# Optimization experiments

Measured on AMD Instinct MI355X. Metric: run time of the kernel, lower is better.

## Reference

```python
import jax, jax.numpy as jnp
import numpy as np

N, M, D0, D1, H, E = 1024, 4096, 1024, 512, 512, 64
TAU = 0.5


def setup_inputs() -> dict:
    key = jax.random.key(0)
    ks = jax.random.split(key, 24)
    g = lambda k, shape, s=0.05: (jax.random.normal(k, shape, jnp.float32) * s)
    # 0/1 meta-path neighbor incidence matrices, avg degree ~16
    nei0 = (jax.random.uniform(ks[0], (N, M)) < 0.004).astype(jnp.float32)
    nei1 = (jax.random.uniform(ks[1], (N, M)) < 0.004).astype(jnp.float32)
    def norm_adj(k):
        a = (jax.random.uniform(k, (N, N)) < 0.005).astype(jnp.float32) + jnp.eye(N, dtype=jnp.float32)
        return a / a.sum(1, keepdims=True)
    return dict(
        feat0=g(ks[2], (N, D0), 1.0), feat1=g(ks[3], (M, D1), 1.0), feat2=g(ks[4], (M, D1), 1.0),
        mask_feat=g(ks[5], (N, D0), 1.0),
        nei0=nei0, nei1=nei1,
        adj0=norm_adj(ks[6]), adj1=norm_adj(ks[7]),
        madj0=norm_adj(ks[8]), madj1=norm_adj(ks[9]),
        fc0_w=g(ks[10], (D0, H)), fc0_b=jnp.zeros((H,), jnp.float32),
        fc1_w=g(ks[11], (D1, H)), fc1_b=jnp.zeros((H,), jnp.float32),
        fc2_w=g(ks[12], (D1, H)), fc2_b=jnp.zeros((H,), jnp.float32),
        agg0_w=g(ks[13], (H, H)), agg1_w=g(ks[14], (H, H)),
        gcn_w1=g(ks[15], (H, E)), gcn_b1=jnp.zeros((E,), jnp.float32),
        gcn_w2=g(ks[16], (E, E)), gcn_b2=jnp.zeros((E,), jnp.float32),
        att_w=g(ks[17], (E, E)), att_b=jnp.zeros((E,), jnp.float32),
        att_vec=g(ks[18], (E,)),
        proj_w=g(ks[19], (E, E)), proj_b=jnp.zeros((E,), jnp.float32),
        mlp1_w=g(ks[20], (E, 16)), mlp1_b=jnp.zeros((16,), jnp.float32),
        mlp2_w=g(ks[21], (16, 1)), mlp2_b=jnp.zeros((1,), jnp.float32),
    )


def _l2norm(x):
    # F.normalize(dim=1)
    return x / jnp.maximum(jnp.linalg.norm(x, axis=1, keepdims=True), 1e-12)


def reference(feat0, feat1, feat2, mask_feat, nei0, nei1, adj0, adj1, madj0, madj1,
              fc0_w, fc0_b, fc1_w, fc1_b, fc2_w, fc2_b, agg0_w, agg1_w,
              gcn_w1, gcn_b1, gcn_w2, gcn_b2, att_w, att_b, att_vec,
              proj_w, proj_b, mlp1_w, mlp1_b, mlp2_w, mlp2_b):
    elu = jax.nn.elu
    # aggregate_nei_acm (dropout in eval mode => identity)
    h_tar = elu(feat0 @ fc0_w + fc0_b)                       # [N, H]
    h_mask = elu(mask_feat @ fc0_w + fc0_b)                  # [N, H]
    h_nei = [elu(feat1 @ fc1_w + fc1_b), elu(feat2 @ fc2_w + fc2_b)]  # [M, H]
    neis = [nei0, nei1]
    agg_ws = [agg0_w, agg1_w]
    views, masks = [], []
    for i in range(2):
        cnt = jnp.maximum(neis[i].sum(1, keepdims=True), 1.0)  # nei_index_count, clamped >0
        h_agg = (neis[i] @ h_nei[i]) / cnt                     # sparse neighbor mean, [N, H]
        t = h_agg @ agg_ws[i]
        views.append(elu(h_tar + t))
        masks.append(elu(h_mask + t))

    def gcn(x, adj):
        # 2-layer GCN: relu(A X W1 + b1) -> A H W2 + b2
        h = jax.nn.relu(adj @ (x @ gcn_w1) + gcn_b1)
        return adj @ (h @ gcn_w2) + gcn_b2

    mean_adj = (adj0 + adj1) * 0.5                           # torch.stack(adjs).mean(0)
    z_coarse = gcn(h_tar, mean_adj)                          # [N, E]
    # order: Encoder(view_i, adj_i), Encoder(mask_i, mask_adj_i) per i
    h_fine = [gcn(views[0], adj0), gcn(masks[0], madj0),
              gcn(views[1], adj1), gcn(masks[1], madj1)]
    hs = jnp.stack([_l2norm(h) for h in h_fine])             # [V=4, N, E]
    # semantic attention over views
    e = jnp.einsum('vne,e->v', jnp.tanh(hs @ att_w + att_b), att_vec) / hs.shape[1]
    beta = jax.nn.softmax(e)
    z_fine = jnp.einsum('v,vne->ne', beta, hs)               # [N, E]
    zc = _l2norm(jnp.tanh(z_coarse @ proj_w + proj_b))
    zf = _l2norm(jnp.tanh(z_fine @ proj_w + proj_b))
    # weight_InfoNce
    logits = (zf @ zc.T) / TAU                               # [N, N]
    dots = jnp.exp(logits)
    pair = zf[:, None, :] + zc[None, :, :]                   # [N, N, E] = z_anchor[i] + z[j]
    w = jax.nn.sigmoid(jnp.tanh(pair @ mlp1_w + mlp1_b) @ mlp2_w + mlp2_b)[..., 0]
    denom = jnp.sum(dots * w, axis=1)
    # -log(diag(dots)/denom) = log(denom) - diag(logits)
    loss = jnp.mean(jnp.log(denom) - jnp.diagonal(logits))
    return loss
```

## Files before the change

### kernel.cpp

```cpp
#include <hip/hip_runtime.h>

#define ACT_NONE 0
#define ACT_ELU  1
#define ACT_RELU 2
#define ACT_TANH 3

typedef __attribute__((ext_vector_type(8))) short short8;
typedef __attribute__((ext_vector_type(4))) float f32x4;

__device__ __forceinline__ float frcp(float x) { return __builtin_amdgcn_rcpf(x); }
__device__ __forceinline__ float fexp(float x) { return __expf(x); }
__device__ __forceinline__ float ftanh(float x) {
    return 1.f - 2.f * frcp(fexp(2.f * x) + 1.f);
}
__device__ __forceinline__ float fsigmoid(float x) {
    return frcp(1.f + fexp(-x));
}

__device__ __forceinline__ float apply_act(float v, int act) {
    if (act == ACT_ELU)  return v > 0.f ? v : fexp(v) - 1.f;
    if (act == ACT_RELU) return fmaxf(v, 0.f);
    if (act == ACT_TANH) return ftanh(v);
    return v;
}

__device__ __forceinline__ unsigned short f2bf(float f) {
    unsigned int u = __float_as_uint(f);
    unsigned int r = (u + 0x7fffu + ((u >> 16) & 1u)) >> 16;
    return (unsigned short)r;
}
__device__ __forceinline__ float bf2f(unsigned short u) {
    return __uint_as_float(((unsigned int)u) << 16);
}

struct CMDesc { const float* in; unsigned short* out; int start4; };
struct CMArr { CMDesc d[6]; int n; int total4; };

__global__ __launch_bounds__(256) void cast_multi_kernel(CMArr a) {
    int g4 = blockIdx.x * 256 + threadIdx.x;
    if (g4 >= a.total4) return;
    int s = 0;
    while (s + 1 < a.n && g4 >= a.d[s + 1].start4) ++s;
    int l4 = g4 - a.d[s].start4;
    float4 v = *reinterpret_cast<const float4*>(a.d[s].in + (size_t)l4 * 4);
    ushort4 o;
    o.x = f2bf(v.x); o.y = f2bf(v.y); o.z = f2bf(v.z); o.w = f2bf(v.w);
    *reinterpret_cast<ushort4*>(a.d[s].out + (size_t)l4 * 4) = o;
}

struct CTDesc { const float* in; unsigned short* out; int R, C, tcols, tile0; };
struct CTArr { CTDesc d[10]; int n; };

__global__ void castT_multi_kernel(CTArr a) {
    int b = blockIdx.x, s = 0;
    while (s + 1 < a.n && b >= a.d[s + 1].tile0) ++s;
    const CTDesc d = a.d[s];
    int lt = b - d.tile0;
    int tr = lt / d.tcols, tc = lt % d.tcols;
    int r0 = tr * 32, c0 = tc * 32;
    __shared__ float t[32][33];
    int tx = threadIdx.x, ty = threadIdx.y;
    for (int i = ty; i < 32; i += 8) {
        int r = r0 + i, c = c0 + tx;
        t[i][tx] = (r < d.R && c < d.C) ? d.in[(size_t)r * d.C + c] : 0.f;
    }
    __syncthreads();
    for (int i = ty; i < 32; i += 8) {
        int c = c0 + i, r = r0 + tx;
        if (c < d.C && r < d.R) d.out[(size_t)c * d.R + r] = f2bf(t[tx][i]);
    }
}

__global__ __launch_bounds__(256) void gemm_bf16_kernel(
    const unsigned short* __restrict__ A, const unsigned short* __restrict__ Bt,
    const unsigned short* __restrict__ Bt2, int m_split,
    const float* __restrict__ bias, const float* __restrict__ bias2,
    float* __restrict__ C, unsigned short* __restrict__ Cbf, int cbf_mlimit,
    int M, int K, int N, int act) {
    const int tid = threadIdx.x;
    const int w = tid >> 6, lane = tid & 63;
    const int wr = w >> 1, wc = w & 1;
    const int lr = lane & 15, lk = lane >> 4;
    const int bm = blockIdx.y * 64, bn = blockIdx.x * 64;
    const unsigned short* Bu = Bt;
    const float* bu = bias;
    if (bm >= m_split) { Bu = Bt2; bu = bias2; }

    const int arow0 = bm + wr * 32 + lr;
    const int brow0 = bn + wc * 32 + lr;

    f32x4 acc[2][2] = {};
    const short8 zero8 = {};
    #pragma unroll 4
    for (int k0 = 0; k0 < K; k0 += 32) {
        short8 a[2], b[2];
        #pragma unroll
        for (int i = 0; i < 2; ++i)
            a[i] = *reinterpret_cast<const short8*>(&A[(size_t)(arow0 + i * 16) * K + k0 + lk * 8]);
        #pragma unroll
        for (int j = 0; j < 2; ++j) {
            int br = brow0 + j * 16;
            b[j] = (br < N) ? *reinterpret_cast<const short8*>(&Bu[(size_t)br * K + k0 + lk * 8])
                            : zero8;
        }
        #pragma unroll
        for (int i = 0; i < 2; ++i)
            #pragma unroll
            for (int j = 0; j < 2; ++j)
                acc[i][j] = __builtin_amdgcn_mfma_f32_16x16x32_bf16(a[i], b[j], acc[i][j], 0, 0, 0);
    }
    #pragma unroll
    for (int i = 0; i < 2; ++i) {
        #pragma unroll
        for (int j = 0; j < 2; ++j) {
            int gcol = bn + wc * 32 + j * 16 + lr;
            if (gcol >= N) continue;
            float bv = bu ? bu[gcol] : 0.f;
            #pragma unroll
            for (int r = 0; r < 4; ++r) {
                int grow = bm + wr * 32 + i * 16 + lk * 4 + r;
                float v = apply_act(acc[i][j][r] + bv, act);
                if (C)   C[(size_t)grow * N + gcol] = v;
                if (Cbf && grow < cbf_mlimit) Cbf[(size_t)grow * N + gcol] = f2bf(v);
            }
        }
    }
}

__global__ __launch_bounds__(256) void neiagg_kernel(
    const float* __restrict__ nei0, const float* __restrict__ nei1,
    const unsigned short* __restrict__ hn0, const unsigned short* __restrict__ hn1,
    unsigned short* __restrict__ hagg) {
    const int row = blockIdx.x, br = blockIdx.y, t = threadIdx.x;
    const float* nei = br ? nei1 : nei0;
    const unsigned short* hn = br ? hn1 : hn0;
    __shared__ int idxs[256];
    __shared__ int cnt;
    if (t == 0) cnt = 0;
    __syncthreads();
    const float4* nr = reinterpret_cast<const float4*>(nei + (size_t)row * 4096);
    for (int j = t; j < 1024; j += 256) {
        float4 v = nr[j];
        if (v.x != 0.f) { int s = atomicAdd(&cnt, 1); if (s < 256) idxs[s] = j * 4 + 0; }
        if (v.y != 0.f) { int s = atomicAdd(&cnt, 1); if (s < 256) idxs[s] = j * 4 + 1; }
        if (v.z != 0.f) { int s = atomicAdd(&cnt, 1); if (s < 256) idxs[s] = j * 4 + 2; }
        if (v.w != 0.f) { int s = atomicAdd(&cnt, 1); if (s < 256) idxs[s] = j * 4 + 3; }
    }
    __syncthreads();
    int n = cnt < 256 ? cnt : 256;
    float inv = frcp(fmaxf((float)cnt, 1.f));
    int c = t * 2;
    float a0 = 0.f, a1 = 0.f, b0 = 0.f, b1 = 0.f;
    int k = 0;
    for (; k + 2 <= n; k += 2) {
        ushort2 u = *reinterpret_cast<const ushort2*>(&hn[(size_t)idxs[k] * 512 + c]);
        ushort2 v = *reinterpret_cast<const ushort2*>(&hn[(size_t)idxs[k + 1] * 512 + c]);
        a0 += bf2f(u.x); a1 += bf2f(u.y);
        b0 += bf2f(v.x); b1 += bf2f(v.y);
    }
    if (k < n) {
        ushort2 u = *reinterpret_cast<const ushort2*>(&hn[(size_t)idxs[k] * 512 + c]);
        a0 += bf2f(u.x); a1 += bf2f(u.y);
    }
    ushort2 o; o.x = f2bf((a0 + b0) * inv); o.y = f2bf((a1 + b1) * inv);
    *reinterpret_cast<ushort2*>(&hagg[((size_t)br * 1024 + row) * 512 + c]) = o;
}

__global__ void addelu_kernel(const float* __restrict__ ht, const float* __restrict__ hm,
                              const float* __restrict__ tt, unsigned short* __restrict__ xcat,
                              int nh) {
    int idx = blockIdx.x * 256 + threadIdx.x;
    if (idx < nh) {
        float h1 = ht[idx], h2 = hm[idx];
        float t0 = tt[idx], t1 = tt[idx + nh];
        float a = h1 + t0, b = h2 + t0, c = h1 + t1, d = h2 + t1;
        xcat[(size_t)1 * nh + idx] = f2bf(a > 0.f ? a : fexp(a) - 1.f);
        xcat[(size_t)2 * nh + idx] = f2bf(b > 0.f ? b : fexp(b) - 1.f);
        xcat[(size_t)3 * nh + idx] = f2bf(c > 0.f ? c : fexp(c) - 1.f);
        xcat[(size_t)4 * nh + idx] = f2bf(d > 0.f ? d : fexp(d) - 1.f);
    }
}

__global__ __launch_bounds__(64) void adjprep_kernel(
    const float* __restrict__ adj0, const float* __restrict__ adj1,
    const float* __restrict__ madj0, const float* __restrict__ madj1,
    int* __restrict__ cnts, int* __restrict__ idxs, float* __restrict__ wts) {
    const int row = blockIdx.x, br = blockIdx.y, t = threadIdx.x;
    const float* Aa; const float* Ab = nullptr; float sc = 1.f;
    if (br == 0)      { Aa = adj0; Ab = adj1; sc = 0.5f; }
    else if (br == 1) { Aa = adj0; }
    else if (br == 2) { Aa = madj0; }
    else if (br == 3) { Aa = adj1; }
    else              { Aa = madj1; }
    __shared__ int li[128];
    __shared__ float lw[128];
    __shared__ int cnt;
    if (t == 0) cnt = 0;
    __syncthreads();
    const float4* ar = reinterpret_cast<const float4*>(Aa + (size_t)row * 1024);
    const float4* brp = Ab ? reinterpret_cast<const float4*>(Ab + (size_t)row * 1024) : nullptr;
    for (int j = t; j < 256; j += 64) {
        float4 v = ar[j];
        if (brp) { float4 u = brp[j]; v.x += u.x; v.y += u.y; v.z += u.z; v.w += u.w; }
        if (v.x != 0.f) { int s = atomicAdd(&cnt, 1); if (s < 128) { li[s] = j * 4 + 0; lw[s] = v.x * sc; } }
        if (v.y != 0.f) { int s = atomicAdd(&cnt, 1); if (s < 128) { li[s] = j * 4 + 1; lw[s] = v.y * sc; } }
        if (v.z != 0.f) { int s = atomicAdd(&cnt, 1); if (s < 128) { li[s] = j * 4 + 2; lw[s] = v.z * sc; } }
        if (v.w != 0.f) { int s = atomicAdd(&cnt, 1); if (s < 128) { li[s] = j * 4 + 3; lw[s] = v.w * sc; } }
    }
    __syncthreads();
    int n = cnt < 128 ? cnt : 128;
    size_t base = ((size_t)br * 1024 + row) * 128;
    for (int k = t; k < n; k += 64) { idxs[base + k] = li[k]; wts[base + k] = lw[k]; }
    if (t == 0) cnts[br * 1024 + row] = n;
}

__device__ __forceinline__ float sparse_gather(const int* __restrict__ idxs,
                                               const float* __restrict__ wts,
                                               size_t base, int n,
                                               const float* __restrict__ Xb, int t,
                                               float acc) {
    float a1 = 0.f, a2 = 0.f, a3 = 0.f;
    int k = 0;
    for (; k + 4 <= n; k += 4) {
        int   i0 = idxs[base + k],     i1 = idxs[base + k + 1];
        int   i2 = idxs[base + k + 2], i3 = idxs[base + k + 3];
        float w0 = wts[base + k],      w1 = wts[base + k + 1];
        float w2 = wts[base + k + 2],  w3 = wts[base + k + 3];
        acc += w0 * Xb[(size_t)i0 * 64 + t];
        a1  += w1 * Xb[(size_t)i1 * 64 + t];
        a2  += w2 * Xb[(size_t)i2 * 64 + t];
        a3  += w3 * Xb[(size_t)i3 * 64 + t];
    }
    for (; k < n; ++k) acc += wts[base + k] * Xb[(size_t)idxs[base + k] * 64 + t];
    return acc + a1 + a2 + a3;
}

__global__ __launch_bounds__(64) void spmm1_kernel(
    const int* __restrict__ cnts, const int* __restrict__ idxs, const float* __restrict__ wts,
    const float* __restrict__ X, const float* __restrict__ bias,
    unsigned short* __restrict__ out) {
    const int row = blockIdx.x, br = blockIdx.y, t = threadIdx.x;
    size_t base = ((size_t)br * 1024 + row) * 128;
    int n = cnts[br * 1024 + row];
    float acc = sparse_gather(idxs, wts, base, n, X + (size_t)br * 1024 * 64, t, bias[t]);
    out[((size_t)br * 1024 + row) * 64 + t] = f2bf(fmaxf(acc, 0.f));
}

__global__ __launch_bounds__(64) void spmm2_kernel(
    const int* __restrict__ cnts, const int* __restrict__ idxs, const float* __restrict__ wts,
    const float* __restrict__ X, const float* __restrict__ bias,
    unsigned short* __restrict__ zcf_bf, float* __restrict__ hs,
    const float* __restrict__ att_w, const float* __restrict__ att_b,
    const float* __restrict__ att_vec, float* __restrict__ att_row) {
    const int row = blockIdx.x, br = blockIdx.y, t = threadIdx.x;
    size_t base = ((size_t)br * 1024 + row) * 128;
    int n = cnts[br * 1024 + row];
    float acc = sparse_gather(idxs, wts, base, n, X + (size_t)br * 1024 * 64, t, bias[t]);
    if (br == 0) {
        zcf_bf[(size_t)row * 64 + t] = f2bf(acc);
        return;
    }
    float s = acc * acc;
    #pragma unroll
    for (int o = 32; o; o >>= 1) s += __shfl_down(s, o);
    s = __shfl(s, 0);
    float v = acc * frcp(fmaxf(sqrtf(s), 1e-12f));
    hs[((size_t)(br - 1) * 1024 + row) * 64 + t] = v;
    __shared__ float rs[64];
    rs[t] = v;
    __syncthreads();
    float sa = att_b[t];
    #pragma unroll
    for (int k = 0; k < 64; ++k) sa += rs[k] * att_w[k * 64 + t];
    float val = ftanh(sa) * att_vec[t];
    #pragma unroll
    for (int o = 32; o; o >>= 1) val += __shfl_down(val, o);
    if (t == 0) att_row[(size_t)(br - 1) * 1024 + row] = val;
}

__global__ __launch_bounds__(256) void attreduce_kernel(const float* __restrict__ att_row,
                                                        float* __restrict__ small) {
    const int v = blockIdx.x, t = threadIdx.x;
    const float* p = att_row + (size_t)v * 1024;
    float s = p[t] + p[t + 256] + p[t + 512] + p[t + 768];
    #pragma unroll
    for (int o = 32; o; o >>= 1) s += __shfl_down(s, o);
    __shared__ float ps[4];
    if ((t & 63) == 0) ps[t >> 6] = s;
    __syncthreads();
    if (t == 0) small[v] = ps[0] + ps[1] + ps[2] + ps[3];
}

__global__ void zfine_kernel(const float* __restrict__ hs, const float* __restrict__ small,
                             unsigned short* __restrict__ out) {
    int idx = blockIdx.x * 256 + threadIdx.x;
    if (idx < 65536) {
        float e0 = small[0] * (1.f / 1024.f), e1 = small[1] * (1.f / 1024.f);
        float e2 = small[2] * (1.f / 1024.f), e3 = small[3] * (1.f / 1024.f);
        float mx = fmaxf(fmaxf(e0, e1), fmaxf(e2, e3));
        float x0 = expf(e0 - mx), x1 = expf(e1 - mx), x2 = expf(e2 - mx), x3 = expf(e3 - mx);
        float inv = 1.f / (x0 + x1 + x2 + x3);
        float v = (x0 * hs[idx] + x1 * hs[idx + 65536] +
                   x2 * hs[idx + 131072] + x3 * hs[idx + 196608]) * inv;
        out[idx] = f2bf(v);
    }
}

__global__ __launch_bounds__(64) void l2normcast_kernel(float* __restrict__ X,
                                                        unsigned short* __restrict__ Xbf) {
    const int row = blockIdx.x, t = threadIdx.x;
    float v = X[(size_t)row * 64 + t];
    float s = v * v;
    #pragma unroll
    for (int o = 32; o; o >>= 1) s += __shfl_down(s, o);
    s = __shfl(s, 0);
    float r = v * frcp(fmaxf(sqrtf(s), 1e-12f));
    X[(size_t)row * 64 + t] = r;
    Xbf[(size_t)row * 64 + t] = f2bf(r);
}

__global__ __launch_bounds__(256) void infonce_kernel(
    const float* __restrict__ zf, const float* __restrict__ zc,
    const float* __restrict__ A1, const float* __restrict__ C1,
    const float* __restrict__ b1, const float* __restrict__ m2,
    const float* __restrict__ b2v, float* __restrict__ loss_acc) {
    const int i0 = blockIdx.x * 4, t = threadIdx.x;
    __shared__ __align__(16) float zfs[4][64];
    __shared__ float a1b[4][16], m2s[16];
    __shared__ float diag[4];
    __shared__ float wsum[4][4];
    if (t < 64) {
        #pragma unroll
        for (int ii = 0; ii < 4; ++ii) zfs[ii][t] = zf[(size_t)(i0 + ii) * 64 + t];
    }
    if (t < 16) {
        float bb = b1[t];
        #pragma unroll
        for (int ii = 0; ii < 4; ++ii) a1b[ii][t] = A1[(size_t)(i0 + ii) * 16 + t] + bb;
        m2s[t] = m2[t];
    }
    __syncthreads();
    const float b2 = b2v[0];
    float acc[4] = {};
    for (int j = t; j < 1024; j += 256) {
        const float4* zcj = reinterpret_cast<const float4*>(zc + (size_t)j * 64);
        float dot[4] = {};
        #pragma unroll
        for (int e = 0; e < 16; ++e) {
            float4 b = zcj[e];
            #pragma unroll
            for (int ii = 0; ii < 4; ++ii) {
                float4 a = reinterpret_cast<const float4*>(zfs[ii])[e];
                dot[ii] += a.x * b.x + a.y * b.y + a.z * b.z + a.w * b.w;
            }
        }
        float c1j[16];
        #pragma unroll
        for (int q = 0; q < 4; ++q) {
            float4 c4 = reinterpret_cast<const float4*>(C1 + (size_t)j * 16)[q];
            c1j[q * 4 + 0] = c4.x; c1j[q * 4 + 1] = c4.y;
            c1j[q * 4 + 2] = c4.z; c1j[q * 4 + 3] = c4.w;
        }
        #pragma unroll
        for (int ii = 0; ii < 4; ++ii) {
            float logit = dot[ii] * 2.0f;
            float h = b2;
            #pragma unroll
            for (int k = 0; k < 16; ++k) h += ftanh(a1b[ii][k] + c1j[k]) * m2s[k];
            acc[ii] += fexp(logit) * fsigmoid(h);
            if (j == i0 + ii) diag[ii] = logit;
        }
    }
    #pragma unroll
    for (int ii = 0; ii < 4; ++ii) {
        float a = acc[ii];
        #pragma unroll
        for (int o = 32; o; o >>= 1) a += __shfl_down(a, o);
        if ((t & 63) == 0) wsum[t >> 6][ii] = a;
    }
    __syncthreads();
    if (t == 0) {
        float part = 0.f;
        #pragma unroll
        for (int ii = 0; ii < 4; ++ii) {
            float denom = wsum[0][ii] + wsum[1][ii] + wsum[2][ii] + wsum[3][ii];
            part += logf(denom) - diag[ii];
        }
        atomicAdd(loss_acc, part);
    }
}

__global__ void finalize_kernel(const float* __restrict__ small, float* __restrict__ out) {
    if (threadIdx.x == 0) out[0] = small[4] * (1.f / 1024.f);
}

extern "C" void kernel_launch(void* const* d_in, const int* in_sizes, int n_in,
                              void* d_out, int out_size, void* d_ws, size_t ws_size,
                              hipStream_t stream) {
    const float* feat0     = (const float*)d_in[0];
    const float* feat1     = (const float*)d_in[1];
    const float* feat2     = (const float*)d_in[2];
    const float* mask_feat = (const float*)d_in[3];
    const float* nei0      = (const float*)d_in[4];
    const float* nei1      = (const float*)d_in[5];
    const float* adj0      = (const float*)d_in[6];
    const float* adj1      = (const float*)d_in[7];
    const float* madj0     = (const float*)d_in[8];
    const float* madj1     = (const float*)d_in[9];
    const float* fc0_w = (const float*)d_in[10];
    const float* fc0_b = (const float*)d_in[11];
    const float* fc1_w = (const float*)d_in[12];
    const float* fc1_b = (const float*)d_in[13];
    const float* fc2_w = (const float*)d_in[14];
    const float* fc2_b = (const float*)d_in[15];
    const float* agg0_w = (const float*)d_in[16];
    const float* agg1_w = (const float*)d_in[17];
    const float* gcn_w1 = (const float*)d_in[18];
    const float* gcn_b1 = (const float*)d_in[19];
    const float* gcn_w2 = (const float*)d_in[20];
    const float* gcn_b2 = (const float*)d_in[21];
    const float* att_w  = (const float*)d_in[22];
    const float* att_b  = (const float*)d_in[23];
    const float* att_vec = (const float*)d_in[24];
    const float* proj_w = (const float*)d_in[25];
    const float* proj_b = (const float*)d_in[26];
    const float* mlp1_w = (const float*)d_in[27];
    const float* mlp1_b = (const float*)d_in[28];
    const float* mlp2_w = (const float*)d_in[29];
    const float* mlp2_b = (const float*)d_in[30];

    const int N = 1024, M = 4096, D0 = 1024, D1 = 512, H = 512, E = 64;
    typedef unsigned short bf;

    float* W = (float*)d_ws;
    size_t off = 0;
    auto allocf = [&](size_t n) { float* p = W + off; off += n; return p; };
    float* h_tar   = allocf((size_t)N * H);
    float* h_mask  = allocf((size_t)N * H);
    float* tbuf    = allocf((size_t)2 * N * H);
    float* xw1cat  = allocf((size_t)5 * N * E);
    float* hw2cat  = allocf((size_t)5 * N * E);
    float* hs      = allocf((size_t)4 * N * E);
    float* zcat    = allocf((size_t)2 * N * E);
    float* AC1     = allocf((size_t)2 * N * 16);
    float* att_row = allocf((size_t)4 * N);
    float* small   = allocf(16);
    float* adj_wts = allocf((size_t)5 * 1024 * 128);
    int*   adj_idx = (int*)allocf((size_t)5 * 1024 * 128);
    int*   adj_cnt = (int*)allocf((size_t)5 * 1024);
    bf* BP = (bf*)(W + off);
    size_t boff = 0;
    auto allocb = [&](size_t n) { bf* p = BP + boff; boff += n; return p; };
    bf* feat0_bf = allocb((size_t)N * D0);
    bf* mask_bf  = allocb((size_t)N * D0);
    bf* feat1_bf = allocb((size_t)M * D1);
    bf* feat2_bf = allocb((size_t)M * D1);
    bf* xcat_bf  = allocb((size_t)5 * N * H);
    bf* hnei0_bf = allocb((size_t)M * H);
    bf* hnei1_bf = allocb((size_t)M * H);
    bf* hagg_bf  = allocb((size_t)2 * N * H);
    bf* h1cat_bf = allocb((size_t)5 * N * E);
    bf* zcf_bf   = allocb((size_t)2 * N * E);
    bf* zcat_bf  = allocb((size_t)2 * N * E);
    bf* fc0_wT  = allocb((size_t)H * D0);
    bf* fc1_wT  = allocb((size_t)H * D1);
    bf* fc2_wT  = allocb((size_t)H * D1);
    bf* agg0_wT = allocb((size_t)H * H);
    bf* agg1_wT = allocb((size_t)H * H);
    bf* gw1_T   = allocb((size_t)E * H);
    bf* gw2_T   = allocb((size_t)E * E);
    bf* proj_wT = allocb((size_t)E * E);
    bf* mlp1_wT = allocb((size_t)16 * E);

    auto gemm = [&](const bf* A, const bf* Bt, const bf* Bt2, int msplit,
                    const float* bias, const float* bias2, float* C, bf* Cbf, int cbf_lim,
                    int Mm, int Kk, int Nn, int act) {
        dim3 g((Nn + 63) / 64, Mm / 64);
        gemm_bf16_kernel<<<g, 256, 0, stream>>>(A, Bt, Bt2, msplit, bias, bias2,
                                                C, Cbf, cbf_lim, Mm, Kk, Nn, act);
    };

    hipMemsetAsync((void*)small, 0, 16 * sizeof(float), stream);

    {
        CTArr a; int tile = 0, i = 0;
        auto add = [&](const float* in, bf* out, int R, int C) {
            int tc = (C + 31) / 32, trn = (R + 31) / 32;
            a.d[i++] = CTDesc{in, out, R, C, tc, tile};
            tile += tc * trn;
        };
        add(fc0_w, fc0_wT, D0, H);
        add(fc1_w, fc1_wT, D1, H);
        add(fc2_w, fc2_wT, D1, H);
        add(agg0_w, agg0_wT, H, H);
        add(agg1_w, agg1_wT, H, H);
        add(gcn_w1, gw1_T, H, E);
        add(gcn_w2, gw2_T, E, E);
        add(proj_w, proj_wT, E, E);
        add(mlp1_w, mlp1_wT, E, 16);
        a.n = i;
        castT_multi_kernel<<<tile, dim3(32, 8), 0, stream>>>(a);
    }
    {
        CMArr a; int s4 = 0, i = 0;
        auto add = [&](const float* in, bf* out, int n) {
            a.d[i++] = CMDesc{in, out, s4}; s4 += n / 4;
        };
        add(feat0, feat0_bf, N * D0);
        add(mask_feat, mask_bf, N * D0);
        add(feat1, feat1_bf, M * D1);
        add(feat2, feat2_bf, M * D1);
        a.n = i; a.total4 = s4;
        cast_multi_kernel<<<(s4 + 255) / 256, 256, 0, stream>>>(a);
    }
    adjprep_kernel<<<dim3(N, 5), 64, 0, stream>>>(adj0, adj1, madj0, madj1,
                                                  adj_cnt, adj_idx, adj_wts);

    gemm(feat0_bf, fc0_wT, nullptr, 1 << 30, fc0_b, nullptr,
         h_tar, xcat_bf, N, 2 * N, D0, H, ACT_ELU);
    gemm(feat1_bf, fc1_wT, fc2_wT, M, fc1_b, fc2_b,
         nullptr, hnei0_bf, 2 * M, 2 * M, D1, H, ACT_ELU);

    neiagg_kernel<<<dim3(N, 2), 256, 0, stream>>>(nei0, nei1, hnei0_bf, hnei1_bf, hagg_bf);
    gemm(hagg_bf, agg0_wT, agg1_wT, N, nullptr, nullptr,
         tbuf, nullptr, 0, 2 * N, H, H, ACT_NONE);
    addelu_kernel<<<(N * H + 255) / 256, 256, 0, stream>>>(h_tar, h_mask, tbuf, xcat_bf, N * H);

    gemm(xcat_bf, gw1_T, nullptr, 1 << 30, nullptr, nullptr,
         xw1cat, nullptr, 0, 5 * N, H, E, ACT_NONE);
    spmm1_kernel<<<dim3(N, 5), 64, 0, stream>>>(adj_cnt, adj_idx, adj_wts, xw1cat, gcn_b1, h1cat_bf);
    gemm(h1cat_bf, gw2_T, nullptr, 1 << 30, nullptr, nullptr,
         hw2cat, nullptr, 0, 5 * N, E, E, ACT_NONE);
    spmm2_kernel<<<dim3(N, 5), 64, 0, stream>>>(adj_cnt, adj_idx, adj_wts, hw2cat, gcn_b2,
                                                zcf_bf, hs, att_w, att_b, att_vec, att_row);
    attreduce_kernel<<<4, 256, 0, stream>>>(att_row, small);

    zfine_kernel<<<(N * E + 255) / 256, 256, 0, stream>>>(hs, small, zcf_bf + (size_t)N * E);

    gemm(zcf_bf, proj_wT, nullptr, 1 << 30, proj_b, nullptr,
         zcat, nullptr, 0, 2 * N, E, E, ACT_TANH);
    l2normcast_kernel<<<2 * N, 64, 0, stream>>>(zcat, zcat_bf);

    gemm(zcat_bf, mlp1_wT, nullptr, 1 << 30, nullptr, nullptr,
         AC1, nullptr, 0, 2 * N, E, 16, ACT_NONE);
    const float* zc = zcat;
    const float* zf = zcat + (size_t)N * E;
    const float* C1 = AC1;
    const float* A1 = AC1 + (size_t)N * 16;
    infonce_kernel<<<N / 4, 256, 0, stream>>>(zf, zc, A1, C1, mlp1_b, mlp2_w, mlp2_b, small + 4);

    finalize_kernel<<<1, 64, 0, stream>>>(small, (float*)d_out);
}
```

Before: 311.7 us.

## Add LDS-staged 128x128 GEMM, merge cast kernels, fuse mlp1 into l2norm

Adds a 128x128-tile GEMM that stages A and B through LDS with global_load_lds for the large H-wide GEMMs, so each fetched tile is reused across more MFMAs. The two cast kernels are merged into one launch. The mlp1 projection is folded into the l2-normalize kernel, which removes a GEMM launch and a bf16 intermediate buffer. SpMM and l2norm kernels now run 4 rows per 256-thread block. The new GEMM assumes M and N are divisible by 128 and has no overlap between loads and compute, and the small per-row mlp1 dot is done on only 16 threads.

```diff
diff --git a/kernel.cpp b/kernel.cpp
--- a/kernel.cpp
+++ b/kernel.cpp
@@ -33,48 +33,117 @@
     return __uint_as_float(((unsigned int)u) << 16);
 }
 
+#define GLOAD16(gp, lp) __builtin_amdgcn_global_load_lds( \
+    (const __attribute__((address_space(1))) void*)(gp),  \
+    (__attribute__((address_space(3))) void*)(lp), 16, 0, 0)
+
+struct CTDesc { const float* in; unsigned short* out; int R, C, tcols, tile0; };
 struct CMDesc { const float* in; unsigned short* out; int start4; };
-struct CMArr { CMDesc d[6]; int n; int total4; };
-
-__global__ __launch_bounds__(256) void cast_multi_kernel(CMArr a) {
-    int g4 = blockIdx.x * 256 + threadIdx.x;
-    if (g4 >= a.total4) return;
-    int s = 0;
-    while (s + 1 < a.n && g4 >= a.d[s + 1].start4) ++s;
-    int l4 = g4 - a.d[s].start4;
-    float4 v = *reinterpret_cast<const float4*>(a.d[s].in + (size_t)l4 * 4);
-    ushort4 o;
-    o.x = f2bf(v.x); o.y = f2bf(v.y); o.z = f2bf(v.z); o.w = f2bf(v.w);
-    *reinterpret_cast<ushort4*>(a.d[s].out + (size_t)l4 * 4) = o;
-}
-
-struct CTDesc { const float* in; unsigned short* out; int R, C, tcols, tile0; };
-struct CTArr { CTDesc d[10]; int n; };
-
-__global__ void castT_multi_kernel(CTArr a) {
-    int b = blockIdx.x, s = 0;
-    while (s + 1 < a.n && b >= a.d[s + 1].tile0) ++s;
-    const CTDesc d = a.d[s];
-    int lt = b - d.tile0;
-    int tr = lt / d.tcols, tc = lt % d.tcols;
-    int r0 = tr * 32, c0 = tc * 32;
-    __shared__ float t[32][33];
-    int tx = threadIdx.x, ty = threadIdx.y;
-    for (int i = ty; i < 32; i += 8) {
-        int r = r0 + i, c = c0 + tx;
-        t[i][tx] = (r < d.R && c < d.C) ? d.in[(size_t)r * d.C + c] : 0.f;
-    }
-    __syncthreads();
-    for (int i = ty; i < 32; i += 8) {
-        int c = c0 + i, r = r0 + tx;
-        if (c < d.C && r < d.R) d.out[(size_t)c * d.R + r] = f2bf(t[tx][i]);
-    }
-}
-
-__global__ __launch_bounds__(256) void gemm_bf16_kernel(
+struct CastArr {
+    CTDesc t[10]; int nt; int T;
+    CMDesc f[6]; int nf; int total4;
+};
+
+__global__ __launch_bounds__(256) void cast_all_kernel(CastArr a) {
+    int b = blockIdx.x;
+    if (b < a.T) {
+        int s = 0;
+        while (s + 1 < a.nt && b >= a.t[s + 1].tile0) ++s;
+        const CTDesc d = a.t[s];
+        int lt = b - d.tile0;
+        int tr = lt / d.tcols, tc = lt % d.tcols;
+        int r0 = tr * 32, c0 = tc * 32;
+        __shared__ float tt[32][33];
+        int tx = threadIdx.x & 31, ty = threadIdx.x >> 5;
+        for (int i = ty; i < 32; i += 8) {
+            int r = r0 + i, c = c0 + tx;
+            tt[i][tx] = (r < d.R && c < d.C) ? d.in[(size_t)r * d.C + c] : 0.f;
+        }
+        __syncthreads();
+        for (int i = ty; i < 32; i += 8) {
+            int c = c0 + i, r = r0 + tx;
+            if (c < d.C && r < d.R) d.out[(size_t)c * d.R + r] = f2bf(tt[tx][i]);
+        }
+    } else {
+        int g4 = (b - a.T) * 256 + threadIdx.x;
+        if (g4 >= a.total4) return;
+        int s = 0;
+        while (s + 1 < a.nf && g4 >= a.f[s + 1].start4) ++s;
+        int l4 = g4 - a.f[s].start4;
+        float4 v = *reinterpret_cast<const float4*>(a.f[s].in + (size_t)l4 * 4);
+        ushort4 o;
+        o.x = f2bf(v.x); o.y = f2bf(v.y); o.z = f2bf(v.z); o.w = f2bf(v.w);
+        *reinterpret_cast<ushort4*>(a.f[s].out + (size_t)l4 * 4) = o;
+    }
+}
+
+__global__ __launch_bounds__(256) void gemm128_kernel(
     const unsigned short* __restrict__ A, const unsigned short* __restrict__ Bt,
     const unsigned short* __restrict__ Bt2, int m_split,
     const float* __restrict__ bias, const float* __restrict__ bias2,
+    float* __restrict__ C, unsigned short* __restrict__ Cbf, int cbf_mlimit,
+    int M, int K, int N, int act) {
+    __shared__ unsigned short As[8 * 512];
+    __shared__ unsigned short Bs[8 * 512];
+    const int tid = threadIdx.x;
+    const int w = tid >> 6, lane = tid & 63;
+    const int wr = w >> 1, wc = w & 1;
+    const int lr = lane & 15, lk = lane >> 4;
+    const int bm = blockIdx.y * 128, bn = blockIdx.x * 128;
+    const unsigned short* Bu = Bt;
+    const float* bu = bias;
+    if (bm >= m_split) { Bu = Bt2; bu = bias2; }
+
+    const unsigned short* ga0 = A  + (size_t)(bm + (2 * w)     * 16 + lr) * K + lk * 8;
+    const unsigned short* ga1 = A  + (size_t)(bm + (2 * w + 1) * 16 + lr) * K + lk * 8;
+    const unsigned short* gb0 = Bu + (size_t)(bn + (2 * w)     * 16 + lr) * K + lk * 8;
+    const unsigned short* gb1 = Bu + (size_t)(bn + (2 * w + 1) * 16 + lr) * K + lk * 8;
+    unsigned short* la0 = &As[(2 * w) * 512];
+    unsigned short* la1 = &As[(2 * w + 1) * 512];
+    unsigned short* lb0 = &Bs[(2 * w) * 512];
+    unsigned short* lb1 = &Bs[(2 * w + 1) * 512];
+
+    f32x4 acc[4][4] = {};
+    for (int k0 = 0; k0 < K; k0 += 32) {
+        GLOAD16(ga0 + k0, la0);
+        GLOAD16(ga1 + k0, la1);
+        GLOAD16(gb0 + k0, lb0);
+        GLOAD16(gb1 + k0, lb1);
+        __syncthreads();
+        short8 a[4], b[4];
+        #pragma unroll
+        for (int i = 0; i < 4; ++i)
+            a[i] = *reinterpret_cast<const short8*>(&As[(4 * wr + i) * 512 + lane * 8]);
+        #pragma unroll
+        for (int j = 0; j < 4; ++j)
+            b[j] = *reinterpret_cast<const short8*>(&Bs[(4 * wc + j) * 512 + lane * 8]);
+        #pragma unroll
+        for (int i = 0; i < 4; ++i)
+            #pragma unroll
+            for (int j = 0; j < 4; ++j)
+                acc[i][j] = __builtin_amdgcn_mfma_f32_16x16x32_bf16(a[i], b[j], acc[i][j], 0, 0, 0);
+        __syncthreads();
+    }
+    #pragma unroll
+    for (int i = 0; i < 4; ++i) {
+        #pragma unroll
+        for (int j = 0; j < 4; ++j) {
+            int gcol = bn + wc * 64 + j * 16 + lr;
+            float bv = bu ? bu[gcol] : 0.f;
+            #pragma unroll
+            for (int r = 0; r < 4; ++r) {
+                int grow = bm + wr * 64 + i * 16 + lk * 4 + r;
+                float v = apply_act(acc[i][j][r] + bv, act);
+                if (C)   C[(size_t)grow * N + gcol] = v;
+                if (Cbf && grow < cbf_mlimit) Cbf[(size_t)grow * N + gcol] = f2bf(v);
+            }
+        }
+    }
+}
+
+__global__ __launch_bounds__(256) void gemm_bf16_kernel(
+    const unsigned short* __restrict__ A, const unsigned short* __restrict__ Bt,
+    const float* __restrict__ bias,
     float* __restrict__ C, unsigned short* __restrict__ Cbf, int cbf_mlimit,
     int M, int K, int N, int act) {
     const int tid = threadIdx.x;
@@ -82,9 +151,6 @@
     const int wr = w >> 1, wc = w & 1;
     const int lr = lane & 15, lk = lane >> 4;
     const int bm = blockIdx.y * 64, bn = blockIdx.x * 64;
-    const unsigned short* Bu = Bt;
-    const float* bu = bias;
-    if (bm >= m_split) { Bu = Bt2; bu = bias2; }
 
     const int arow0 = bm + wr * 32 + lr;
     const int brow0 = bn + wc * 32 + lr;
@@ -100,7 +166,7 @@
         #pragma unroll
         for (int j = 0; j < 2; ++j) {
             int br = brow0 + j * 16;
-            b[j] = (br < N) ? *reinterpret_cast<const short8*>(&Bu[(size_t)br * K + k0 + lk * 8])
+            b[j] = (br < N) ? *reinterpret_cast<const short8*>(&Bt[(size_t)br * K + k0 + lk * 8])
                             : zero8;
         }
         #pragma unroll
@@ -115,7 +181,7 @@
         for (int j = 0; j < 2; ++j) {
             int gcol = bn + wc * 32 + j * 16 + lr;
             if (gcol >= N) continue;
-            float bv = bu ? bu[gcol] : 0.f;
+            float bv = bias ? bias[gcol] : 0.f;
             #pragma unroll
             for (int r = 0; r < 4; ++r) {
                 int grow = bm + wr * 32 + i * 16 + lk * 4 + r;
@@ -235,24 +301,27 @@
     return acc + a1 + a2 + a3;
 }
 
-__global__ __launch_bounds__(64) void spmm1_kernel(
+__global__ __launch_bounds__(256) void spmm1_kernel(
     const int* __restrict__ cnts, const int* __restrict__ idxs, const float* __restrict__ wts,
     const float* __restrict__ X, const float* __restrict__ bias,
     unsigned short* __restrict__ out) {
-    const int row = blockIdx.x, br = blockIdx.y, t = threadIdx.x;
+    const int row = blockIdx.x * 4 + (threadIdx.x >> 6);
+    const int br = blockIdx.y, t = threadIdx.x & 63;
     size_t base = ((size_t)br * 1024 + row) * 128;
     int n = cnts[br * 1024 + row];
     float acc = sparse_gather(idxs, wts, base, n, X + (size_t)br * 1024 * 64, t, bias[t]);
     out[((size_t)br * 1024 + row) * 64 + t] = f2bf(fmaxf(acc, 0.f));
 }
 
-__global__ __launch_bounds__(64) void spmm2_kernel(
+__global__ __launch_bounds__(256) void spmm2_kernel(
     const int* __restrict__ cnts, const int* __restrict__ idxs, const float* __restrict__ wts,
     const float* __restrict__ X, const float* __restrict__ bias,
     unsigned short* __restrict__ zcf_bf, float* __restrict__ hs,
     const float* __restrict__ att_w, const float* __restrict__ att_b,
     const float* __restrict__ att_vec, float* __restrict__ att_row) {
-    const int row = blockIdx.x, br = blockIdx.y, t = threadIdx.x;
+    const int wv = threadIdx.x >> 6;
+    const int row = blockIdx.x * 4 + wv;
+    const int br = blockIdx.y, t = threadIdx.x & 63;
     size_t base = ((size_t)br * 1024 + row) * 128;
     int n = cnts[br * 1024 + row];
     float acc = sparse_gather(idxs, wts, base, n, X + (size_t)br * 1024 * 64, t, bias[t]);
@@ -266,12 +335,11 @@
     s = __shfl(s, 0);
     float v = acc * frcp(fmaxf(sqrtf(s), 1e-12f));
     hs[((size_t)(br - 1) * 1024 + row) * 64 + t] = v;
-    __shared__ float rs[64];
-    rs[t] = v;
-    __syncthreads();
+    __shared__ float rs[4][64];
+    rs[wv][t] = v;
     float sa = att_b[t];
     #pragma unroll
-    for (int k = 0; k < 64; ++k) sa += rs[k] * att_w[k * 64 + t];
+    for (int k = 0; k < 64; ++k) sa += rs[wv][k] * att_w[k * 64 + t];
     float val = ftanh(sa) * att_vec[t];
     #pragma unroll
     for (int o = 32; o; o >>= 1) val += __shfl_down(val, o);
@@ -306,9 +374,12 @@
     }
 }
 
-__global__ __launch_bounds__(64) void l2normcast_kernel(float* __restrict__ X,
-                                                        unsigned short* __restrict__ Xbf) {
-    const int row = blockIdx.x, t = threadIdx.x;
+__global__ __launch_bounds__(256) void l2normA1_kernel(float* __restrict__ X,
+                                                       const unsigned short* __restrict__ mlp1_wT,
+                                                       float* __restrict__ AC1) {
+    const int wv = threadIdx.x >> 6;
+    const int row = blockIdx.x * 4 + wv;
+    const int t = threadIdx.x & 63;
     float v = X[(size_t)row * 64 + t];
     float s = v * v;
     #pragma unroll
@@ -316,7 +387,14 @@
     s = __shfl(s, 0);
     float r = v * frcp(fmaxf(sqrtf(s), 1e-12f));
     X[(size_t)row * 64 + t] = r;
-    Xbf[(size_t)row * 64 + t] = f2bf(r);
+    __shared__ float zs[4][64];
+    zs[wv][t] = r;
+    if (t < 16) {
+        float acc = 0.f;
+        #pragma unroll
+        for (int e = 0; e < 64; ++e) acc += zs[wv][e] * bf2f(mlp1_wT[t * 64 + e]);
+        AC1[(size_t)row * 16 + t] = acc;
+    }
 }
 
 __global__ __launch_bounds__(256) void infonce_kernel(
@@ -461,7 +539,6 @@
     bf* hagg_bf  = allocb((size_t)2 * N * H);
     bf* h1cat_bf = allocb((size_t)5 * N * E);
     bf* zcf_bf   = allocb((size_t)2 * N * E);
-    bf* zcat_bf  = allocb((size_t)2 * N * E);
     bf* fc0_wT  = allocb((size_t)H * D0);
     bf* fc1_wT  = allocb((size_t)H * D1);
     bf* fc2_wT  = allocb((size_t)H * D1);
@@ -472,77 +549,75 @@
     bf* proj_wT = allocb((size_t)E * E);
     bf* mlp1_wT = allocb((size_t)16 * E);
 
-    auto gemm = [&](const bf* A, const bf* Bt, const bf* Bt2, int msplit,
-                    const float* bias, const float* bias2, float* C, bf* Cbf, int cbf_lim,
-                    int Mm, int Kk, int Nn, int act) {
+    auto gemm128 = [&](const bf* A, const bf* Bt, const bf* Bt2, int msplit,
+                       const float* bias, const float* bias2, float* C, bf* Cbf, int cbf_lim,
+                       int Mm, int Kk, int Nn, int act) {
+        dim3 g(Nn / 128, Mm / 128);
+        gemm128_kernel<<<g, 256, 0, stream>>>(A, Bt, Bt2, msplit, bias, bias2,
+                                              C, Cbf, cbf_lim, Mm, Kk, Nn, act);
+    };
+    auto gemm64 = [&](const bf* A, const bf* Bt, const float* bias, float* C, bf* Cbf,
+                      int cbf_lim, int Mm, int Kk, int Nn, int act) {
         dim3 g((Nn + 63) / 64, Mm / 64);
-        gemm_bf16_kernel<<<g, 256, 0, stream>>>(A, Bt, Bt2, msplit, bias, bias2,
-                                                C, Cbf, cbf_lim, Mm, Kk, Nn, act);
+        gemm_bf16_kernel<<<g, 256, 0, stream>>>(A, Bt, bias, C, Cbf, cbf_lim, Mm, Kk, Nn, act);
     };
 
     hipMemsetAsync((void*)small, 0, 16 * sizeof(float), stream);
 
     {
-        CTArr a; int tile = 0, i = 0;
-        auto add = [&](const float* in, bf* out, int R, int C) {
+        CastArr a; int tile = 0, i = 0;
+        auto addT = [&](const float* in, bf* out, int R, int C) {
             int tc = (C + 31) / 32, trn = (R + 31) / 32;
-            a.d[i++] = CTDesc{in, out, R, C, tc, tile};
+            a.t[i++] = CTDesc{in, out, R, C, tc, tile};
             tile += tc * trn;
         };
-        add(fc0_w, fc0_wT, D0, H);
-        add(fc1_w, fc1_wT, D1, H);
-        add(fc2_w, fc2_wT, D1, H);
-        add(agg0_w, agg0_wT, H, H);
-        add(agg1_w, agg1_wT, H, H);
-        add(gcn_w1, gw1_T, H, E);
-        add(gcn_w2, gw2_T, E, E);
-        add(proj_w, proj_wT, E, E);
-        add(mlp1_w, mlp1_wT, E, 16);
-        a.n = i;
-        castT_multi_kernel<<<tile, dim3(32, 8), 0, stream>>>(a);
-    }
-    {
-        CMArr a; int s4 = 0, i = 0;
-        auto add = [&](const float* in, bf* out, int n) {
-            a.d[i++] = CMDesc{in, out, s4}; s4 += n / 4;
+        addT(fc0_w, fc0_wT, D0, H);
+        addT(fc1_w, fc1_wT, D1, H);
+        addT(fc2_w, fc2_wT, D1, H);
+        addT(agg0_w, agg0_wT, H, H);
+        addT(agg1_w, agg1_wT, H, H);
+        addT(gcn_w1, gw1_T, H, E);
+        addT(gcn_w2, gw2_T, E, E);
+        addT(proj_w, proj_wT, E, E);
+        addT(mlp1_w, mlp1_wT, E, 16);
+        a.nt = i; a.T = tile;
+        int s4 = 0, fi = 0;
+        auto addF = [&](const float* in, bf* out, int n) {
+            a.f[fi++] = CMDesc{in, out, s4}; s4 += n / 4;
         };
-        add(feat0, feat0_bf, N * D0);
-        add(mask_feat, mask_bf, N * D0);
-        add(feat1, feat1_bf, M * D1);
-        add(feat2, feat2_bf, M * D1);
-        a.n = i; a.total4 = s4;
-        cast_multi_kernel<<<(s4 + 255) / 256, 256, 0, stream>>>(a);
+        addF(feat0, feat0_bf, N * D0);
+        addF(mask_feat, mask_bf, N * D0);
+        addF(feat1, feat1_bf, M * D1);
+        addF(feat2, feat2_bf, M * D1);
+        a.nf = fi; a.total4 = s4;
+        int nb = tile + (s4 + 255) / 256;
+        cast_all_kernel<<<nb, 256, 0, stream>>>(a);
     }
     adjprep_kernel<<<dim3(N, 5), 64, 0, stream>>>(adj0, adj1, madj0, madj1,
                                                   adj_cnt, adj_idx, adj_wts);
 
-    gemm(feat0_bf, fc0_wT, nullptr, 1 << 30, fc0_b, nullptr,
-         h_tar, xcat_bf, N, 2 * N, D0, H, ACT_ELU);
-    gemm(feat1_bf, fc1_wT, fc2_wT, M, fc1_b, fc2_b,
-         nullptr, hnei0_bf, 2 * M, 2 * M, D1, H, ACT_ELU);
+    gemm128(feat0_bf, fc0_wT, nullptr, 1 << 30, fc0_b, nullptr,
+            h_tar, xcat_bf, N, 2 * N, D0, H, ACT_ELU);
+    gemm128(feat1_bf, fc1_wT, fc2_wT, M, fc1_b, fc2_b,
+            nullptr, hnei0_bf, 2 * M, 2 * M, D1, H, ACT_ELU);
 
     neiagg_kernel<<<dim3(N, 2), 256, 0, stream>>>(nei0, nei1, hnei0_bf, hnei1_bf, hagg_bf);
-    gemm(hagg_bf, agg0_wT, agg1_wT, N, nullptr, nullptr,
-         tbuf, nullptr, 0, 2 * N, H, H, ACT_NONE);
+    gemm128(hagg_bf, agg0_wT, agg1_wT, N, nullptr, nullptr,
+            tbuf, nullptr, 0, 2 * N, H, H, ACT_NONE);
     addelu_kernel<<<(N * H + 255) / 256, 256, 0, stream>>>(h_tar, h_mask, tbuf, xcat_bf, N * H);
 
-    gemm(xcat_bf, gw1_T, nullptr, 1 << 30, nullptr, nullptr,
-         xw1cat, nullptr, 0, 5 * N, H, E, ACT_NONE);
-    spmm1_kernel<<<dim3(N, 5), 64, 0, stream>>>(adj_cnt, adj_idx, adj_wts, xw1cat, gcn_b1, h1cat_bf);
-    gemm(h1cat_bf, gw2_T, nullptr, 1 << 30, nullptr, nullptr,
-         hw2cat, nullptr, 0, 5 * N, E, E, ACT_NONE);
-    spmm2_kernel<<<dim3(N, 5), 64, 0, stream>>>(adj_cnt, adj_idx, adj_wts, hw2cat, gcn_b2,
-                                                zcf_bf, hs, att_w, att_b, att_vec, att_row);
+    gemm64(xcat_bf, gw1_T, nullptr, xw1cat, nullptr, 0, 5 * N, H, E, ACT_NONE);
+    spmm1_kernel<<<dim3(N / 4, 5), 256, 0, stream>>>(adj_cnt, adj_idx, adj_wts, xw1cat, gcn_b1, h1cat_bf);
+    gemm64(h1cat_bf, gw2_T, nullptr, hw2cat, nullptr, 0, 5 * N, E, E, ACT_NONE);
+    spmm2_kernel<<<dim3(N / 4, 5), 256, 0, stream>>>(adj_cnt, adj_idx, adj_wts, hw2cat, gcn_b2,
+                                                     zcf_bf, hs, att_w, att_b, att_vec, att_row);
     attreduce_kernel<<<4, 256, 0, stream>>>(att_row, small);
 
     zfine_kernel<<<(N * E + 255) / 256, 256, 0, stream>>>(hs, small, zcf_bf + (size_t)N * E);
 
-    gemm(zcf_bf, proj_wT, nullptr, 1 << 30, proj_b, nullptr,
-         zcat, nullptr, 0, 2 * N, E, E, ACT_TANH);
-    l2normcast_kernel<<<2 * N, 64, 0, stream>>>(zcat, zcat_bf);
-
-    gemm(zcat_bf, mlp1_wT, nullptr, 1 << 30, nullptr, nullptr,
-         AC1, nullptr, 0, 2 * N, E, 16, ACT_NONE);
+    gemm64(zcf_bf, proj_wT, proj_b, zcat, nullptr, 0, 2 * N, E, E, ACT_TANH);
+    l2normA1_kernel<<<2 * N / 4, 256, 0, stream>>>(zcat, mlp1_wT, AC1);
+
     const float* zc = zcat;
     const float* zf = zcat + (size_t)N * E;
     const float* C1 = AC1;
```

New measurement: 325.4 us. 1.04x slower.
